# Optimization experiments

Hardware: AMD Instinct MI355X
Metric: run time of the kernel (lower is better)

The kernel has to match this reference:

```python
import jax, jax.numpy as jnp
import numpy as np

B, N, C, E, H, V, T = 64, 196, 512, 512, 1024, 10000, 20
NULL_IDX, START_IDX = 0, 1


def setup_inputs() -> dict:
    key = jax.random.key(0)
    ks = jax.random.split(key, 16)
    p = lambda k, s: jax.random.normal(k, s, jnp.float32) * 0.02
    z = lambda n: jnp.zeros((n,), jnp.float32)
    return dict(
        X=jax.random.normal(ks[0], (B, N, C), jnp.float32),
        emb=p(ks[1], (V, E)),
        W_ih=p(ks[2], (E + C, 4 * H)), b_ih=z(4 * H),
        W_hh=p(ks[3], (H, 4 * H)), b_hh=z(4 * H),
        Wa=p(ks[4], (C, H)), ba=z(H),          # attention lin_annotations
        Wh=p(ks[5], (H, H)), bh=z(H),          # attention lin_hidden
        Wo=p(ks[6], (H, 1)), bo=z(1),          # attention out
        Wlh=p(ks[7], (H, E)), blh=z(E),        # linear_hidden
        Wlc=p(ks[8], (C, E)), blc=z(E),        # linear_context
        Wout=p(ks[9], (E, V)), bout=z(V),      # linear_out
        Wc0=p(ks[10], (C, H)), bc0=z(H),       # cell_init
        Wh0=p(ks[11], (C, H)), bh0=z(H),       # hidden_init
    )


def reference(X, emb, W_ih, b_ih, W_hh, b_hh, Wa, ba, Wh, bh, Wo, bo,
              Wlh, blh, Wlc, blc, Wout, bout, Wc0, bc0, Wh0, bh0):
    Xm = jnp.mean(X, axis=1)                       # [B, C]
    c0 = jnp.tanh(Xm @ Wc0 + bc0)                  # [B, H]
    h0 = jnp.tanh(Xm @ Wh0 + bh0)                  # [B, H]
    Xa = X @ Wa + ba                               # [B, N, H] step-invariant annotation proj
    tok0 = jnp.full((B,), START_IDX, jnp.int32)

    def step(carry, _):
        tok, h, c = carry
        e = emb[tok]                                           # [B, E]
        att = jnp.tanh(Xa + (h @ Wh + bh)[:, None, :])          # [B, N, H]
        # softmax over a size-1 last axis -> weights == 1 (faithful to original)
        w = jax.nn.softmax(att @ Wo + bo, axis=-1)              # [B, N, 1]
        ctx = jnp.sum(w * X, axis=1)                            # [B, C]
        gates = jnp.concatenate([e, ctx], axis=1) @ W_ih + b_ih + h @ W_hh + b_hh
        gi, gf, gg, go = jnp.split(gates, 4, axis=1)            # torch LSTMCell gate order
        c2 = jax.nn.sigmoid(gf) * c + jax.nn.sigmoid(gi) * jnp.tanh(gg)
        h2 = jax.nn.sigmoid(go) * jnp.tanh(c2)
        comb = e + (h2 @ Wlh + blh) + (ctx @ Wlc + blc)         # [B, E]
        lp = jax.nn.log_softmax(comb @ Wout + bout, axis=-1)    # [B, V]
        tok2 = jnp.argmax(lp, axis=-1).astype(jnp.int32)
        return (tok2, h2, c2), lp

    _, lps = jax.lax.scan(step, (tok0, h0, c0), None, length=T - 1)  # [T-1, B, V]
    out0 = jnp.broadcast_to(jax.nn.one_hot(START_IDX, V, dtype=jnp.float32), (B, V))[None]
    out = jnp.concatenate([out0, lps], axis=0)                  # [T, B, V]
    return jnp.transpose(out, (1, 0, 2))                        # [B, T, V]
```

## Files before the change

### kernel.cpp

```cpp
#include <hip/hip_runtime.h>
#include <math.h>

typedef unsigned short u16;
typedef unsigned long long u64;
typedef __attribute__((ext_vector_type(8))) short bf16x8;
typedef __attribute__((ext_vector_type(4))) float f32x4;
typedef __attribute__((ext_vector_type(8))) unsigned short ushort8;

constexpr int kB = 64;
constexpr int kN = 196;
constexpr int kC = 512;
constexpr int kE = 512;
constexpr int kH = 1024;
constexpr int kV = 10000;
constexpr int kT = 20;
constexpr int kG4 = 4 * kH;
constexpr int kKA = 1536;
constexpr int kLT = 625;

__device__ __forceinline__ float sigmoidf_(float x) { return 1.0f / (1.0f + expf(-x)); }

__device__ __forceinline__ u16 f2bf(float x) {
    unsigned u = __float_as_uint(x);
    u += 0x7FFF + ((u >> 16) & 1);
    return (u16)(u >> 16);
}
__device__ __forceinline__ float bf2f(u16 u) {
    return __uint_as_float((unsigned)u << 16);
}
__device__ __forceinline__ void splitbf(float x, u16& hi, u16& lo) {
    hi = f2bf(x);
    lo = f2bf(x - bf2f(hi));
}

__device__ __forceinline__ u64 packMI(float M, int I) {
    unsigned mb = __float_as_uint(M);
    mb = (mb & 0x80000000u) ? ~mb : (mb | 0x80000000u);
    return ((u64)mb << 32) | (u64)(0xFFFFFFFFu - (unsigned)I);
}


__global__ __launch_bounds__(256) void k_colsum(const float* __restrict__ X,
                                                float* __restrict__ XsP) {
    int gid = blockIdx.x * 256 + threadIdx.x;
    int c = gid & 511, b = (gid >> 9) & 63, ch = gid >> 15;
    const float* p = X + (size_t)b * kN * kC + (size_t)(ch * 49) * kC + c;
    float s = 0.f;
    for (int n = 0; n < 49; ++n) s += p[(size_t)n * kC];
    XsP[gid] = s;
}

__global__ __launch_bounds__(256) void k_colred(const float* __restrict__ XsP,
                                                float* __restrict__ XsT) {
    int gid = blockIdx.x * 256 + threadIdx.x;
    int b = gid >> 9, c = gid & 511;
    float s = 0.f;
#pragma unroll
    for (int ch = 0; ch < 4; ++ch) s += XsP[ch * 32768 + b * 512 + c];
    XsT[c * kB + b] = s;
}

__global__ __launch_bounds__(256) void k_setupgemm(const float* __restrict__ XsT,
                                                   const float* __restrict__ W_ih,
                                                   const float* __restrict__ b_ih,
                                                   const float* __restrict__ b_hh,
                                                   const float* __restrict__ Wc0,
                                                   const float* __restrict__ bc0,
                                                   const float* __restrict__ Wh0,
                                                   const float* __restrict__ bh0,
                                                   const float* __restrict__ Wlc,
                                                   const float* __restrict__ blc,
                                                   const float* __restrict__ blh,
                                                   float* __restrict__ gbP,
                                                   float* __restrict__ cBJ,
                                                   u16* __restrict__ hb0Hi,
                                                   u16* __restrict__ hb0Lo,
                                                   float* __restrict__ ctxc) {
    __shared__ float4 wt4[64][8];
    int t = threadIdx.x;
    int b = t & 63, q = t >> 6;
    int tile = blockIdx.x;

    const float* W; const float* bias; float scale; int ldw; int mode; int j;
    if (tile < 128) {
        j = tile * 32; W = W_ih + (size_t)kE * kG4 + j; ldw = kG4;
        bias = nullptr; scale = 1.f; mode = 0;
    } else if (tile < 160) {
        j = (tile - 128) * 32; W = Wc0 + j; ldw = kH;
        bias = bc0 + j; scale = 1.0f / 196.0f; mode = 1;
    } else if (tile < 192) {
        j = (tile - 160) * 32; W = Wh0 + j; ldw = kH;
        bias = bh0 + j; scale = 1.0f / 196.0f; mode = 2;
    } else {
        j = (tile - 192) * 32; W = Wlc + j; ldw = kE;
        bias = blc + j; scale = 1.f; mode = 3;
    }

    int lr = t >> 2, lq2 = (t & 3) * 2;
    float acc[8];
#pragma unroll
    for (int i = 0; i < 8; ++i) acc[i] = 0.f;

    for (int kt = 0; kt < kC; kt += 64) {
        const float* wrow = W + (size_t)(kt + lr) * ldw;
        float4 w0 = *reinterpret_cast<const float4*>(wrow + lq2 * 4);
        float4 w1 = *reinterpret_cast<const float4*>(wrow + lq2 * 4 + 4);
        __syncthreads();
        wt4[lr][lq2] = w0; wt4[lr][lq2 + 1] = w1;
        __syncthreads();
        const float* ap = XsT + (size_t)kt * kB + b;
#pragma unroll 8
        for (int kk = 0; kk < 64; ++kk) {
            float a = ap[kk * 64] * scale;
            float4 u0 = wt4[kk][q * 2];
            float4 u1 = wt4[kk][q * 2 + 1];
            acc[0] += a * u0.x; acc[1] += a * u0.y; acc[2] += a * u0.z; acc[3] += a * u0.w;
            acc[4] += a * u1.x; acc[5] += a * u1.y; acc[6] += a * u1.z; acc[7] += a * u1.w;
        }
    }
#pragma unroll
    for (int cc = 0; cc < 8; ++cc) {
        int col = q * 8 + cc;
        float v = acc[cc];
        if (mode == 0) {
            int jsrc = j + col;
            v += b_ih[jsrc] + b_hh[jsrc];
            int nd = ((jsrc & 1023) << 2) | (jsrc >> 10);
            gbP[(size_t)b * kG4 + nd] = v;
        } else if (mode == 1) {
            v = tanhf(v + bias[col]);
            cBJ[(size_t)b * kH + j + col] = v;
        } else if (mode == 2) {
            v = tanhf(v + bias[col]);
            u16 hi, lo; splitbf(v, hi, lo);
            hb0Hi[(size_t)b * kH + j + col] = hi;
            hb0Lo[(size_t)b * kH + j + col] = lo;
        } else {
            v += bias[col] + blh[j + col];
            ctxc[(size_t)b * kE + j + col] = v;
        }
    }
}

__global__ __launch_bounds__(256) void k_wconv(const float* __restrict__ src,
                                               u16* __restrict__ dhi,
                                               u16* __restrict__ dlo,
                                               int ld, int n_valid, int pitch,
                                               int k_off, int nxTiles) {
    __shared__ float lds[64][65];
    int t = threadIdx.x;
    int nx = blockIdx.x % nxTiles, ky = blockIdx.x / nxTiles;
    int n0 = nx * 64, k0 = ky * 64;
    int c = t & 63, r0 = t >> 6;
#pragma unroll
    for (int i = 0; i < 16; ++i) {
        int r = r0 + i * 4;
        float v = (n0 + c < n_valid) ? src[(size_t)(k0 + r) * ld + n0 + c] : 0.f;
        lds[r][c] = v;
    }
    __syncthreads();
    int nl = t >> 2, kq = t & 3;
#pragma unroll
    for (int half = 0; half < 2; ++half) {
        ushort8 vh, vl;
#pragma unroll
        for (int jj = 0; jj < 8; ++jj) {
            u16 hi, lo; splitbf(lds[kq * 16 + half * 8 + jj][nl], hi, lo);
            vh[jj] = hi; vl[jj] = lo;
        }
        size_t o = (size_t)(n0 + nl) * pitch + k_off + k0 + kq * 16 + half * 8;
        *(ushort8*)(&dhi[o]) = vh;
        *(ushort8*)(&dlo[o]) = vl;
    }
}

__global__ __launch_bounds__(256) void k_wgconv(const float* __restrict__ src,
                                                u16* __restrict__ dhi,
                                                int k_off) {
    __shared__ float lds[64][65];
    int t = threadIdx.x;
    int nx = blockIdx.x & 63, ky = blockIdx.x >> 6;
    int n0 = nx * 64, k0 = ky * 64;
    int c = t & 63, r0 = t >> 6;
#pragma unroll
    for (int i = 0; i < 16; ++i) {
        int r = r0 + i * 4;
        int nd = n0 + c;
        int nsrc = (nd & 3) * 1024 + (nd >> 2);
        lds[r][c] = src[(size_t)(k0 + r) * kG4 + nsrc];
    }
    __syncthreads();
    int nl = t >> 2, kq = t & 3;
#pragma unroll
    for (int half = 0; half < 2; ++half) {
        ushort8 vh;
#pragma unroll
        for (int jj = 0; jj < 8; ++jj) vh[jj] = f2bf(lds[kq * 16 + half * 8 + jj][nl]);
        size_t o = (size_t)(n0 + nl) * kKA + k_off + k0 + kq * 16 + half * 8;
        *(ushort8*)(&dhi[o]) = vh;
    }
}

__global__ __launch_bounds__(256) void k_wconvh(const float* __restrict__ src,
                                                u16* __restrict__ dhi,
                                                int ld, int pitch, int nxTiles) {
    __shared__ float lds[64][65];
    int t = threadIdx.x;
    int nx = blockIdx.x % nxTiles, ky = blockIdx.x / nxTiles;
    int n0 = nx * 64, k0 = ky * 64;
    int c = t & 63, r0 = t >> 6;
#pragma unroll
    for (int i = 0; i < 16; ++i) {
        int r = r0 + i * 4;
        lds[r][c] = src[(size_t)(k0 + r) * ld + n0 + c];
    }
    __syncthreads();
    int nl = t >> 2, kq = t & 3;
#pragma unroll
    for (int half = 0; half < 2; ++half) {
        ushort8 vh;
#pragma unroll
        for (int jj = 0; jj < 8; ++jj) vh[jj] = f2bf(lds[kq * 16 + half * 8 + jj][nl]);
        size_t o = (size_t)(n0 + nl) * pitch + k0 + kq * 16 + half * 8;
        *(ushort8*)(&dhi[o]) = vh;
    }
}

__global__ __launch_bounds__(256) void k_embconv(const float* __restrict__ emb,
                                                 u16* __restrict__ eh,
                                                 u16* __restrict__ el) {
    int gid = blockIdx.x * 256 + threadIdx.x;
    float4 v = *reinterpret_cast<const float4*>(emb + (size_t)gid * 4);
    u16 h0, l0, h1, l1, h2, l2, h3, l3;
    splitbf(v.x, h0, l0); splitbf(v.y, h1, l1);
    splitbf(v.z, h2, l2); splitbf(v.w, h3, l3);
    u64 ph = (u64)h0 | ((u64)h1 << 16) | ((u64)h2 << 32) | ((u64)h3 << 48);
    u64 pl = (u64)l0 | ((u64)l1 << 16) | ((u64)l2 << 32) | ((u64)l3 << 48);
    *reinterpret_cast<u64*>(eh + (size_t)gid * 4) = ph;
    *reinterpret_cast<u64*>(el + (size_t)gid * 4) = pl;
}

__global__ __launch_bounds__(256) void k_out0(float* __restrict__ out) {
    int gid = blockIdx.x * 256 + threadIdx.x;
    if (gid >= kB * kV) return;
    int b = gid / kV, v = gid - b * kV;
    out[(size_t)b * kT * kV + v] = (v == 1) ? 1.0f : 0.0f;
}


struct StepP {
    u16 *hbHi0, *hbLo0, *hbHi1, *hbLo1;
    float *cBJ, *gbP, *ctxc;
    u16 *CbHi, *CbLo;
    const u16 *WgHi, *WlhHi, *WoHi, *WoLo, *embHi, *embLo;
    const float *bout;
    float *lbuf0, *lbuf1;
    float *Ssh;
    u64 *Mxsh;
    float *out;
};

__device__ __forceinline__ int resolveTok(const StepP& p, int step, int b) {
    if (step <= 1) return 1;
    int slot = (step - 1) & 1;
    u64 best = 0;
#pragma unroll
    for (int sh = 0; sh < 8; ++sh) {
        u64 v = p.Mxsh[(slot * 8 + sh) * 64 + b];
        if (v > best) best = v;
    }
    return (int)(0xFFFFFFFFu - (unsigned)(best & 0xFFFFFFFFu));
}

__global__ __launch_bounds__(512) void k_stepG(StepP p, int step) {
    __shared__ float sred[8][64][17];
    __shared__ int tok[64];
    const int blk = blockIdx.x, t = threadIdx.x;
    const int l = t & 63, w = t >> 6, la = l & 15, lg = l >> 4;
    const int Pb = (step - 1) & 1, Qb = step & 1;

    if (t < 64) tok[t] = resolveTok(p, step, t);
    if (blk < 8 && t < 64) {
        int slot = step & 1;
        p.Ssh[(slot * 8 + blk) * 64 + t] = 0.f;
        p.Mxsh[(slot * 8 + blk) * 64 + t] = 0;
    }
    __syncthreads();

    const u16* hpHi = Pb ? p.hbHi1 : p.hbHi0;
    const u16* hpLo = Pb ? p.hbLo1 : p.hbLo0;
    u16* nHi = Qb ? p.hbHi1 : p.hbHi0;
    u16* nLo = Qb ? p.hbLo1 : p.hbLo0;
    const int n0 = blk * 16;
    const int kb = w * 192 + lg * 8;
    const u16* wh = p.WgHi + (size_t)(n0 + la) * kKA + kb;
    int tk[4];
#pragma unroll
    for (int m = 0; m < 4; ++m) tk[m] = tok[m * 16 + la];

    f32x4 acc[4];
#pragma unroll
    for (int m = 0; m < 4; ++m) acc[m] = (f32x4){0.f, 0.f, 0.f, 0.f};
#pragma unroll
    for (int ks = 0; ks < 6; ++ks) {
        int kc = w * 192 + ks * 32;
        bf16x8 bhi = *(const bf16x8*)(wh + ks * 32);
#pragma unroll
        for (int m = 0; m < 4; ++m) {
            int row = m * 16 + la;
            bf16x8 ahi8, alo8;
            if (kc < kE) {
                size_t o = (size_t)tk[m] * kE + kc + lg * 8;
                ahi8 = *(const bf16x8*)(p.embHi + o);
                alo8 = *(const bf16x8*)(p.embLo + o);
            } else {
                size_t o = (size_t)row * kH + (kc - kE) + lg * 8;
                ahi8 = *(const bf16x8*)(hpHi + o);
                alo8 = *(const bf16x8*)(hpLo + o);
            }
            acc[m] = __builtin_amdgcn_mfma_f32_16x16x32_bf16(ahi8, bhi, acc[m], 0, 0, 0);
            acc[m] = __builtin_amdgcn_mfma_f32_16x16x32_bf16(alo8, bhi, acc[m], 0, 0, 0);
        }
    }
#pragma unroll
    for (int m = 0; m < 4; ++m)
#pragma unroll
        for (int r = 0; r < 4; ++r)
            sred[w][m * 16 + lg * 4 + r][la] = acc[m][r];
    __syncthreads();
    if (t < 256) {
        int b = t & 63, jl = (t >> 6) & 3;
        float g[4];
#pragma unroll
        for (int gi = 0; gi < 4; ++gi) {
            int cc = jl * 4 + gi;
            float s = p.gbP[(size_t)b * kG4 + n0 + cc];
#pragma unroll
            for (int wv = 0; wv < 8; ++wv) s += sred[wv][b][cc];
            g[gi] = s;
        }
        int jp = blk * 4 + jl;
        float cold = p.cBJ[b * kH + jp];
        float c2 = sigmoidf_(g[1]) * cold + sigmoidf_(g[0]) * tanhf(g[2]);
        float h2 = sigmoidf_(g[3]) * tanhf(c2);
        p.cBJ[b * kH + jp] = c2;
        u16 hh, hl; splitbf(h2, hh, hl);
        nHi[(size_t)b * kH + jp] = hh;
        nLo[(size_t)b * kH + jp] = hl;
    }
}

__global__ __launch_bounds__(256) void k_stepC(StepP p, int step) {
    __shared__ float sred[4][64][17];
    __shared__ int tok[64];
    __shared__ float lseArr[64];
    const int blk = blockIdx.x, t = threadIdx.x;
    const int Qb = step & 1;

    if (blk < 32) {
        if (t < 64) tok[t] = resolveTok(p, step, t);
        __syncthreads();
        const u16* hcHi = Qb ? p.hbHi1 : p.hbHi0;
        const u16* hcLo = Qb ? p.hbLo1 : p.hbLo0;
        const int l = t & 63, w = t >> 6, la = l & 15, lg = l >> 4;
        const int n0 = blk * 16;
        const int kb = w * 256 + lg * 8;
        const u16* wh = p.WlhHi + (size_t)(n0 + la) * kH + kb;
        f32x4 acc[4];
#pragma unroll
        for (int m = 0; m < 4; ++m) acc[m] = (f32x4){0.f, 0.f, 0.f, 0.f};
        for (int ks = 0; ks < 8; ++ks) {
            int ko = ks * 32;
            bf16x8 bhi = *(const bf16x8*)(wh + ko);
#pragma unroll
            for (int m = 0; m < 4; ++m) {
                size_t o = (size_t)(m * 16 + la) * kH + kb + ko;
                bf16x8 ahi8 = *(const bf16x8*)(hcHi + o);
                bf16x8 alo8 = *(const bf16x8*)(hcLo + o);
                acc[m] = __builtin_amdgcn_mfma_f32_16x16x32_bf16(ahi8, bhi, acc[m], 0, 0, 0);
                acc[m] = __builtin_amdgcn_mfma_f32_16x16x32_bf16(alo8, bhi, acc[m], 0, 0, 0);
            }
        }
#pragma unroll
        for (int m = 0; m < 4; ++m)
#pragma unroll
            for (int r = 0; r < 4; ++r)
                sred[w][m * 16 + lg * 4 + r][la] = acc[m][r];
        __syncthreads();
        int b = t & 63, cq = t >> 6;
        int tokb = tok[b];
#pragma unroll
        for (int i = 0; i < 4; ++i) {
            int cc = cq * 4 + i;
            int col = (blk * 16) + cc;
            float v = sred[0][b][cc] + sred[1][b][cc] + sred[2][b][cc] + sred[3][b][cc];
            v += bf2f(p.embHi[(size_t)tokb * kE + col]) + bf2f(p.embLo[(size_t)tokb * kE + col]);
            v += p.ctxc[(size_t)b * kE + col];
            u16 hh, hl; splitbf(v, hh, hl);
            p.CbHi[(size_t)b * kE + col] = hh;
            p.CbLo[(size_t)b * kE + col] = hl;
        }
    } else if (step > 1) {
        int slot = (step - 1) & 1;
        if (t < 64) {
            float S = 0.f;
#pragma unroll
            for (int sh = 0; sh < 8; ++sh) S += p.Ssh[(slot * 8 + sh) * 64 + t];
            lseArr[t] = logf(S);
        }
        __syncthreads();
        const float* lb = slot ? p.lbuf1 : p.lbuf0;
        for (int idx = (blk - 32) * 256 + t; idx < kB * kV; idx += 224 * 256) {
            int b = idx / kV, c = idx - b * kV;
            __builtin_nontemporal_store(lb[(size_t)b * kV + c] - lseArr[b],
                                        &p.out[((size_t)b * kT + (step - 1)) * kV + c]);
        }
    }
}

__global__ __launch_bounds__(256) void k_stepL(StepP p, int step) {
    __shared__ float sred[4][64][17];
    __shared__ float redM[256], redS[256];
    __shared__ int redI[256];
    const int blk = blockIdx.x, t = threadIdx.x;
    const int l = t & 63, w = t >> 6, la = l & 15, lg = l >> 4;
    int slot = step & 1;
    float* lb = slot ? p.lbuf1 : p.lbuf0;
    int shard = blk & 7;
    const int c0 = blk * 16;
    const int kb = w * 128 + lg * 8;
    const u16* wh = p.WoHi + (size_t)(c0 + la) * kE + kb;
    const u16* wl = p.WoLo + (size_t)(c0 + la) * kE + kb;
    const u16* a0h = p.CbHi + (size_t)la * kE + kb;
    const u16* a0l = p.CbLo + (size_t)la * kE + kb;
    f32x4 acc[4];
#pragma unroll
    for (int m = 0; m < 4; ++m) acc[m] = (f32x4){0.f, 0.f, 0.f, 0.f};
#pragma unroll
    for (int ks = 0; ks < 4; ++ks) {
        int ko = ks * 32;
        bf16x8 bhi = *(const bf16x8*)(wh + ko);
        bf16x8 blo = *(const bf16x8*)(wl + ko);
#pragma unroll
        for (int m = 0; m < 4; ++m) {
            bf16x8 ahi8 = *(const bf16x8*)(a0h + (size_t)m * 16 * kE + ko);
            bf16x8 alo8 = *(const bf16x8*)(a0l + (size_t)m * 16 * kE + ko);
            acc[m] = __builtin_amdgcn_mfma_f32_16x16x32_bf16(ahi8, bhi, acc[m], 0, 0, 0);
            acc[m] = __builtin_amdgcn_mfma_f32_16x16x32_bf16(ahi8, blo, acc[m], 0, 0, 0);
            acc[m] = __builtin_amdgcn_mfma_f32_16x16x32_bf16(alo8, bhi, acc[m], 0, 0, 0);
        }
    }
#pragma unroll
    for (int m = 0; m < 4; ++m)
#pragma unroll
        for (int r = 0; r < 4; ++r)
            sred[w][m * 16 + lg * 4 + r][la] = acc[m][r];
    __syncthreads();
    int b = l, cq = w;
    float vals[4];
#pragma unroll
    for (int i = 0; i < 4; ++i) {
        int cc = cq * 4 + i;
        vals[i] = sred[0][b][cc] + sred[1][b][cc] + sred[2][b][cc] + sred[3][b][cc]
                + p.bout[c0 + cc];
    }
    __builtin_nontemporal_store((f32x4){vals[0], vals[1], vals[2], vals[3]},
                                (f32x4*)(lb + (size_t)b * kV + c0 + cq * 4));
    float m = vals[0]; int mi = 0;
#pragma unroll
    for (int i = 1; i < 4; ++i) if (vals[i] > m) { m = vals[i]; mi = i; }
    float se = 0.f;
#pragma unroll
    for (int i = 0; i < 4; ++i) se += __expf(vals[i] - m);
    redM[t] = m; redS[t] = se; redI[t] = c0 + cq * 4 + mi;
    __syncthreads();
    if (t < 64) {
        float M = redM[t], S = redS[t]; int I = redI[t];
#pragma unroll
        for (int q2 = 1; q2 < 4; ++q2) {
            float m2 = redM[t + q2 * 64], s2 = redS[t + q2 * 64];
            int i2 = redI[t + q2 * 64];
            float Mn = fmaxf(M, m2);
            S = S * __expf(M - Mn) + s2 * __expf(m2 - Mn);
            if (m2 > M || (m2 == M && i2 < I)) I = i2;
            M = Mn;
        }
        float S0 = S * __expf(M);
        atomicAdd(&p.Ssh[(slot * 8 + shard) * 64 + t], S0);
        atomicMax(&p.Mxsh[(slot * 8 + shard) * 64 + t], packMI(M, I));
    }
}

__global__ __launch_bounds__(256) void k_stepO(StepP p) {
    __shared__ float lseArr[64];
    const int blk = blockIdx.x, t = threadIdx.x;
    int slot = (kT - 1) & 1;
    if (t < 64) {
        float S = 0.f;
#pragma unroll
        for (int sh = 0; sh < 8; ++sh) S += p.Ssh[(slot * 8 + sh) * 64 + t];
        lseArr[t] = logf(S);
    }
    __syncthreads();
    const float* lb = slot ? p.lbuf1 : p.lbuf0;
    for (int idx = blk * 256 + t; idx < kB * kV; idx += 256 * 256) {
        int b = idx / kV, c = idx - b * kV;
        __builtin_nontemporal_store(lb[(size_t)b * kV + c] - lseArr[b],
                                    &p.out[((size_t)b * kT + (kT - 1)) * kV + c]);
    }
}


extern "C" void kernel_launch(void* const* d_in, const int* in_sizes, int n_in,
                              void* d_out, int out_size, void* d_ws, size_t ws_size,
                              hipStream_t stream) {
    const float* X    = (const float*)d_in[0];
    const float* emb  = (const float*)d_in[1];
    const float* W_ih = (const float*)d_in[2];
    const float* b_ih = (const float*)d_in[3];
    const float* W_hh = (const float*)d_in[4];
    const float* b_hh = (const float*)d_in[5];
    const float* Wlh  = (const float*)d_in[12];
    const float* blh  = (const float*)d_in[13];
    const float* Wlc  = (const float*)d_in[14];
    const float* blc  = (const float*)d_in[15];
    const float* Wout = (const float*)d_in[16];
    const float* bout = (const float*)d_in[17];
    const float* Wc0  = (const float*)d_in[18];
    const float* bc0  = (const float*)d_in[19];
    const float* Wh0  = (const float*)d_in[20];
    const float* bh0  = (const float*)d_in[21];
    float* out = (float*)d_out;

    char* cur = (char*)d_ws;
    auto carve = [&](size_t bytes) { char* p = cur; cur += (bytes + 255) & ~(size_t)255; return p; };

    u16* hbHi0 = (u16*)carve((size_t)kB * kH * 2);
    u16* hbLo0 = (u16*)carve((size_t)kB * kH * 2);
    u16* hbHi1 = (u16*)carve((size_t)kB * kH * 2);
    u16* hbLo1 = (u16*)carve((size_t)kB * kH * 2);
    float* cBJ  = (float*)carve((size_t)kB * kH * 4);
    float* gbP  = (float*)carve((size_t)kB * kG4 * 4);
    float* ctxc = (float*)carve((size_t)kB * kE * 4);
    u16* CbHi   = (u16*)carve((size_t)kB * kE * 2);
    u16* CbLo   = (u16*)carve((size_t)kB * kE * 2);
    float* XsT  = (float*)carve((size_t)kC * kB * 4);
    float* XsP  = (float*)carve((size_t)4 * kB * kC * 4);
    u16* WgHi   = (u16*)carve((size_t)kG4 * kKA * 2);
    u16* WlhHi  = (u16*)carve((size_t)kE * kH * 2);
    u16* WoHi   = (u16*)carve((size_t)10048 * kE * 2);
    u16* WoLo   = (u16*)carve((size_t)10048 * kE * 2);
    u16* embHi  = (u16*)carve((size_t)10000 * kE * 2);
    u16* embLo  = (u16*)carve((size_t)10000 * kE * 2);
    float* lbuf0 = (float*)carve((size_t)kB * kV * 4);
    float* lbuf1 = (float*)carve((size_t)kB * kV * 4);
    float* Ssh   = (float*)carve((size_t)2 * 8 * 64 * 4);
    u64*   Mxsh  = (u64*)carve((size_t)2 * 8 * 64 * 8);

    k_colsum<<<512, 256, 0, stream>>>(X, XsP);
    k_colred<<<128, 256, 0, stream>>>(XsP, XsT);
    k_setupgemm<<<208, 256, 0, stream>>>(XsT, W_ih, b_ih, b_hh, Wc0, bc0,
                                         Wh0, bh0, Wlc, blc, blh,
                                         gbP, cBJ, hbHi0, hbLo0, ctxc);
    k_out0<<<(kB * kV + 255) / 256, 256, 0, stream>>>(out);
    k_wgconv<<<64 * 8, 256, 0, stream>>>(W_ih, WgHi, 0);
    k_wgconv<<<64 * 16, 256, 0, stream>>>(W_hh, WgHi, kE);
    k_wconvh<<<8 * 16, 256, 0, stream>>>(Wlh, WlhHi, kE, kH, 8);
    k_wconv<<<157 * 8, 256, 0, stream>>>(Wout, WoHi, WoLo, kV, kV, kE, 0, 157);
    k_embconv<<<5000, 256, 0, stream>>>(emb, embHi, embLo);

    StepP sp;
    sp.hbHi0 = hbHi0; sp.hbLo0 = hbLo0; sp.hbHi1 = hbHi1; sp.hbLo1 = hbLo1;
    sp.cBJ = cBJ; sp.gbP = gbP; sp.ctxc = ctxc;
    sp.CbHi = CbHi; sp.CbLo = CbLo;
    sp.WgHi = WgHi; sp.WlhHi = WlhHi;
    sp.WoHi = WoHi; sp.WoLo = WoLo; sp.embHi = embHi; sp.embLo = embLo;
    sp.bout = bout;
    sp.lbuf0 = lbuf0; sp.lbuf1 = lbuf1;
    sp.Ssh = Ssh; sp.Mxsh = Mxsh;
    sp.out = out;

    for (int s = 1; s < kT; ++s) {
        k_stepG<<<256, 512, 0, stream>>>(sp, s);
        k_stepC<<<256, 256, 0, stream>>>(sp, s);
        k_stepL<<<kLT, 256, 0, stream>>>(sp, s);
    }
    k_stepO<<<256, 256, 0, stream>>>(sp);
}
```

Measured before the change: 1.022 ms.

## Fuse combine and logits kernels with an in-kernel atomic counter barrier

Merges the per-step combine kernel (k_stepC) and the vocab-logits kernel (k_stepL) into one launch of 625 blocks. The first 32 blocks compute the combined embedding vector and then bump a global atomic counter. The other blocks either write the previous step's log-softmax output or go straight to spinning until the counter reaches 32*step, then run the logits GEMM. This removes one kernel launch per step and overlaps the output writeback with the counter wait. It also adds nontemporal loads on the lbuf and WoLo streams. The spin-wait relies on the 32 producer blocks being resident alongside the waiters, so it risks deadlock or stalls if they are not scheduled, and its iteration cap could let a block proceed on stale data.

```diff
diff --git a/kernel.cpp b/kernel.cpp
--- a/kernel.cpp
+++ b/kernel.cpp
@@ -37,6 +37,26 @@
     unsigned mb = __float_as_uint(M);
     mb = (mb & 0x80000000u) ? ~mb : (mb | 0x80000000u);
     return ((u64)mb << 32) | (u64)(0xFFFFFFFFu - (unsigned)I);
+}
+
+__device__ __forceinline__ void bumpCtr(int* c) {
+    __syncthreads();
+    if (threadIdx.x == 0) {
+        __builtin_amdgcn_fence(__ATOMIC_RELEASE, "agent");
+        __hip_atomic_fetch_add(c, 1, __ATOMIC_RELAXED, __HIP_MEMORY_SCOPE_AGENT);
+    }
+}
+__device__ __forceinline__ void waitGE(const int* c, int target) {
+    if (threadIdx.x == 0) {
+        int it = 0;
+        while (__hip_atomic_load(c, __ATOMIC_RELAXED, __HIP_MEMORY_SCOPE_AGENT) < target
+               && it < (1 << 20)) {
+            __builtin_amdgcn_s_sleep(8);
+            ++it;
+        }
+        __builtin_amdgcn_fence(__ATOMIC_ACQUIRE, "agent");
+    }
+    __syncthreads();
 }
 
 
@@ -258,6 +278,7 @@
     float *Ssh;
     u64 *Mxsh;
     float *out;
+    int *ctrs;
 };
 
 __device__ __forceinline__ int resolveTok(const StepP& p, int step, int b) {
@@ -350,11 +371,14 @@
     }
 }
 
-__global__ __launch_bounds__(256) void k_stepC(StepP p, int step) {
+__global__ __launch_bounds__(256) void k_stepCL(StepP p, int step) {
     __shared__ float sred[4][64][17];
+    __shared__ float redM[256], redS[256];
+    __shared__ int redI[256];
     __shared__ int tok[64];
     __shared__ float lseArr[64];
     const int blk = blockIdx.x, t = threadIdx.x;
+    const int l = t & 63, w = t >> 6, la = l & 15, lg = l >> 4;
     const int Qb = step & 1;
 
     if (blk < 32) {
@@ -362,7 +386,6 @@
         __syncthreads();
         const u16* hcHi = Qb ? p.hbHi1 : p.hbHi0;
         const u16* hcLo = Qb ? p.hbLo1 : p.hbLo0;
-        const int l = t & 63, w = t >> 6, la = l & 15, lg = l >> 4;
         const int n0 = blk * 16;
         const int kb = w * 256 + lg * 8;
         const u16* wh = p.WlhHi + (size_t)(n0 + la) * kH + kb;
@@ -387,20 +410,23 @@
             for (int r = 0; r < 4; ++r)
                 sred[w][m * 16 + lg * 4 + r][la] = acc[m][r];
         __syncthreads();
-        int b = t & 63, cq = t >> 6;
-        int tokb = tok[b];
-#pragma unroll
-        for (int i = 0; i < 4; ++i) {
-            int cc = cq * 4 + i;
-            int col = (blk * 16) + cc;
-            float v = sred[0][b][cc] + sred[1][b][cc] + sred[2][b][cc] + sred[3][b][cc];
-            v += bf2f(p.embHi[(size_t)tokb * kE + col]) + bf2f(p.embLo[(size_t)tokb * kE + col]);
-            v += p.ctxc[(size_t)b * kE + col];
-            u16 hh, hl; splitbf(v, hh, hl);
-            p.CbHi[(size_t)b * kE + col] = hh;
-            p.CbLo[(size_t)b * kE + col] = hl;
-        }
-    } else if (step > 1) {
+        {
+            int b = t & 63, cq = t >> 6;
+            int tokb = tok[b];
+#pragma unroll
+            for (int i = 0; i < 4; ++i) {
+                int cc = cq * 4 + i;
+                int col = (blk * 16) + cc;
+                float v = sred[0][b][cc] + sred[1][b][cc] + sred[2][b][cc] + sred[3][b][cc];
+                v += bf2f(p.embHi[(size_t)tokb * kE + col]) + bf2f(p.embLo[(size_t)tokb * kE + col]);
+                v += p.ctxc[(size_t)b * kE + col];
+                u16 hh, hl; splitbf(v, hh, hl);
+                p.CbHi[(size_t)b * kE + col] = hh;
+                p.CbLo[(size_t)b * kE + col] = hl;
+            }
+        }
+        bumpCtr(p.ctrs);
+    } else if (blk < 256 && step > 1) {
         int slot = (step - 1) & 1;
         if (t < 64) {
             float S = 0.f;
@@ -412,20 +438,15 @@
         const float* lb = slot ? p.lbuf1 : p.lbuf0;
         for (int idx = (blk - 32) * 256 + t; idx < kB * kV; idx += 224 * 256) {
             int b = idx / kV, c = idx - b * kV;
-            __builtin_nontemporal_store(lb[(size_t)b * kV + c] - lseArr[b],
+            float v = __builtin_nontemporal_load(&lb[(size_t)b * kV + c]);
+            __builtin_nontemporal_store(v - lseArr[b],
                                         &p.out[((size_t)b * kT + (step - 1)) * kV + c]);
         }
     }
-}
-
-__global__ __launch_bounds__(256) void k_stepL(StepP p, int step) {
-    __shared__ float sred[4][64][17];
-    __shared__ float redM[256], redS[256];
-    __shared__ int redI[256];
-    const int blk = blockIdx.x, t = threadIdx.x;
-    const int l = t & 63, w = t >> 6, la = l & 15, lg = l >> 4;
-    int slot = step & 1;
-    float* lb = slot ? p.lbuf1 : p.lbuf0;
+
+    waitGE(p.ctrs, 32 * step);
+
+    float* lb = Qb ? p.lbuf1 : p.lbuf0;
     int shard = blk & 7;
     const int c0 = blk * 16;
     const int kb = w * 128 + lg * 8;
@@ -440,7 +461,7 @@
     for (int ks = 0; ks < 4; ++ks) {
         int ko = ks * 32;
         bf16x8 bhi = *(const bf16x8*)(wh + ko);
-        bf16x8 blo = *(const bf16x8*)(wl + ko);
+        bf16x8 blo = __builtin_nontemporal_load((const bf16x8*)(wl + ko));
 #pragma unroll
         for (int m = 0; m < 4; ++m) {
             bf16x8 ahi8 = *(const bf16x8*)(a0h + (size_t)m * 16 * kE + ko);
@@ -456,23 +477,25 @@
         for (int r = 0; r < 4; ++r)
             sred[w][m * 16 + lg * 4 + r][la] = acc[m][r];
     __syncthreads();
-    int b = l, cq = w;
-    float vals[4];
-#pragma unroll
-    for (int i = 0; i < 4; ++i) {
-        int cc = cq * 4 + i;
-        vals[i] = sred[0][b][cc] + sred[1][b][cc] + sred[2][b][cc] + sred[3][b][cc]
-                + p.bout[c0 + cc];
-    }
-    __builtin_nontemporal_store((f32x4){vals[0], vals[1], vals[2], vals[3]},
-                                (f32x4*)(lb + (size_t)b * kV + c0 + cq * 4));
-    float m = vals[0]; int mi = 0;
-#pragma unroll
-    for (int i = 1; i < 4; ++i) if (vals[i] > m) { m = vals[i]; mi = i; }
-    float se = 0.f;
-#pragma unroll
-    for (int i = 0; i < 4; ++i) se += __expf(vals[i] - m);
-    redM[t] = m; redS[t] = se; redI[t] = c0 + cq * 4 + mi;
+    {
+        int b = l, cq = w;
+        float vals[4];
+#pragma unroll
+        for (int i = 0; i < 4; ++i) {
+            int cc = cq * 4 + i;
+            vals[i] = sred[0][b][cc] + sred[1][b][cc] + sred[2][b][cc] + sred[3][b][cc]
+                    + p.bout[c0 + cc];
+        }
+        __builtin_nontemporal_store((f32x4){vals[0], vals[1], vals[2], vals[3]},
+                                    (f32x4*)(lb + (size_t)b * kV + c0 + cq * 4));
+        float m = vals[0]; int mi = 0;
+#pragma unroll
+        for (int i = 1; i < 4; ++i) if (vals[i] > m) { m = vals[i]; mi = i; }
+        float se = 0.f;
+#pragma unroll
+        for (int i = 0; i < 4; ++i) se += __expf(vals[i] - m);
+        redM[t] = m; redS[t] = se; redI[t] = c0 + cq * 4 + mi;
+    }
     __syncthreads();
     if (t < 64) {
         float M = redM[t], S = redS[t]; int I = redI[t];
@@ -486,6 +509,7 @@
             M = Mn;
         }
         float S0 = S * __expf(M);
+        int slot = step & 1;
         atomicAdd(&p.Ssh[(slot * 8 + shard) * 64 + t], S0);
         atomicMax(&p.Mxsh[(slot * 8 + shard) * 64 + t], packMI(M, I));
     }
@@ -505,7 +529,8 @@
     const float* lb = slot ? p.lbuf1 : p.lbuf0;
     for (int idx = blk * 256 + t; idx < kB * kV; idx += 256 * 256) {
         int b = idx / kV, c = idx - b * kV;
-        __builtin_nontemporal_store(lb[(size_t)b * kV + c] - lseArr[b],
+        float v = __builtin_nontemporal_load(&lb[(size_t)b * kV + c]);
+        __builtin_nontemporal_store(v - lseArr[b],
                                     &p.out[((size_t)b * kT + (kT - 1)) * kV + c]);
     }
 }
@@ -556,6 +581,9 @@
     float* lbuf1 = (float*)carve((size_t)kB * kV * 4);
     float* Ssh   = (float*)carve((size_t)2 * 8 * 64 * 4);
     u64*   Mxsh  = (u64*)carve((size_t)2 * 8 * 64 * 8);
+    int*   ctrs  = (int*)carve(256);
+
+    hipMemsetAsync(ctrs, 0, 256, stream);
 
     k_colsum<<<512, 256, 0, stream>>>(X, XsP);
     k_colred<<<128, 256, 0, stream>>>(XsP, XsT);
@@ -579,11 +607,11 @@
     sp.lbuf0 = lbuf0; sp.lbuf1 = lbuf1;
     sp.Ssh = Ssh; sp.Mxsh = Mxsh;
     sp.out = out;
+    sp.ctrs = ctrs;
 
     for (int s = 1; s < kT; ++s) {
         k_stepG<<<256, 512, 0, stream>>>(sp, s);
-        k_stepC<<<256, 256, 0, stream>>>(sp, s);
-        k_stepL<<<kLT, 256, 0, stream>>>(sp, s);
+        k_stepCL<<<kLT, 256, 0, stream>>>(sp, s);
     }
     k_stepO<<<256, 256, 0, stream>>>(sp);
 }
```

New measurement: 1.139 ms. 1.11x slower.
